# Kernel tuning notes

Measured on AMD Instinct MI355X. Metric: run time of the kernel, lower is better.

The kernel has to match this reference:

```python
import jax, jax.numpy as jnp
from jax import lax
import numpy as np

INPUT_SIZE = 128
T = 64
B = 8192
HIDDENS = [32, 16, 8]
FUTURE = 1


def _lstm_layer(x, w_ih, w_hh, b_ih, b_hh):
    """PyTorch-semantics single-layer LSTM, batch_first, zero init state.
    x: [B,T,D]; w_ih: [4H,D]; w_hh: [4H,H]; b_ih,b_hh: [4H]. Gate order i,f,g,o.
    Returns all hidden states [B,T,H]."""
    Bsz = x.shape[0]
    H = w_hh.shape[1]
    # Precompute input contribution for all timesteps in one big GEMM.
    xg = jnp.einsum('btd,gd->btg', x, w_ih) + b_ih + b_hh  # [B,T,4H]
    xg_t = jnp.swapaxes(xg, 0, 1)  # [T,B,4H]

    def step(carry, xt):
        h, c = carry
        gates = xt + h @ w_hh.T  # [B,4H]
        i, f, g, o = jnp.split(gates, 4, axis=-1)
        i = jax.nn.sigmoid(i)
        f = jax.nn.sigmoid(f)
        g = jnp.tanh(g)
        o = jax.nn.sigmoid(o)
        c = f * c + i * g
        h = o * jnp.tanh(c)
        return (h, c), h

    init = (jnp.zeros((Bsz, H), x.dtype), jnp.zeros((Bsz, H), x.dtype))
    _, hs = lax.scan(step, init, xg_t)  # hs: [T,B,H]
    return jnp.swapaxes(hs, 0, 1)


def setup_inputs() -> dict:
    key = jax.random.key(0)
    ks = jax.random.split(key, 16)
    s = 0.1

    def rn(k, shape):
        return jax.random.normal(k, shape, dtype=jnp.float32) * s

    inp = {
        'x': jax.random.normal(ks[0], (B, T, INPUT_SIZE), dtype=jnp.float32),
        'w_ih1': rn(ks[1], (4 * 32, INPUT_SIZE)),
        'w_hh1': rn(ks[2], (4 * 32, 32)),
        'b_ih1': rn(ks[3], (4 * 32,)),
        'b_hh1': rn(ks[4], (4 * 32,)),
        'w_ih2': rn(ks[5], (4 * 16, 32)),
        'w_hh2': rn(ks[6], (4 * 16, 16)),
        'b_ih2': rn(ks[7], (4 * 16,)),
        'b_hh2': rn(ks[8], (4 * 16,)),
        'w_ih3': rn(ks[9], (4 * 8, 16)),
        'w_hh3': rn(ks[10], (4 * 8, 8)),
        'b_ih3': rn(ks[11], (4 * 8,)),
        'b_hh3': rn(ks[12], (4 * 8,)),
        'fc_w': rn(ks[13], (FUTURE, 8)),
        'fc_b': rn(ks[14], (FUTURE,)),
    }
    return inp


def reference(x, w_ih1, w_hh1, b_ih1, b_hh1, w_ih2, w_hh2, b_ih2, b_hh2,
              w_ih3, w_hh3, b_ih3, b_hh3, fc_w, fc_b):
    h = _lstm_layer(x, w_ih1, w_hh1, b_ih1, b_hh1)   # [B,T,32]
    h = _lstm_layer(h, w_ih2, w_hh2, b_ih2, b_hh2)   # [B,T,16]
    h = _lstm_layer(h, w_ih3, w_hh3, b_ih3, b_hh3)   # [B,T,8]
    return h[:, -1, :] @ fc_w.T + fc_b               # [B, FUTURE]
```

## Files before the change

### kernel.cpp

```cpp
#include <hip/hip_runtime.h>
#include <cstddef>
#include <type_traits>


typedef _Float16 h8_t  __attribute__((ext_vector_type(8)));
typedef _Float16 h4_t  __attribute__((ext_vector_type(4)));
typedef __fp16   p2_t  __attribute__((ext_vector_type(2)));
typedef float    f4_t  __attribute__((ext_vector_type(4)));

#define T_LEN 64
#define D_IN  128

__device__ __forceinline__ float sig_(float x)  { return 1.0f / (1.0f + __expf(-x)); }
__device__ __forceinline__ float tanh_(float x) { float e = __expf(2.0f * x); return 1.0f - 2.0f / (e + 1.0f); }

__device__ __forceinline__ h8_t zero8h() {
    h8_t r = { (_Float16)0.f,(_Float16)0.f,(_Float16)0.f,(_Float16)0.f,
               (_Float16)0.f,(_Float16)0.f,(_Float16)0.f,(_Float16)0.f };
    return r;
}
__device__ __forceinline__ h8_t cvt8(f4_t lo, f4_t hi) {
    union { h8_t v8; p2_t v2[4]; } u;
    u.v2[0] = __builtin_amdgcn_cvt_pkrtz(lo[0], lo[1]);
    u.v2[1] = __builtin_amdgcn_cvt_pkrtz(lo[2], lo[3]);
    u.v2[2] = __builtin_amdgcn_cvt_pkrtz(hi[0], hi[1]);
    u.v2[3] = __builtin_amdgcn_cvt_pkrtz(hi[2], hi[3]);
    return u.v8;
}
__device__ __forceinline__ h4_t cvt4(f4_t v) {
    union { h4_t v4; p2_t v2[2]; } u;
    u.v2[0] = __builtin_amdgcn_cvt_pkrtz(v[0], v[1]);
    u.v2[1] = __builtin_amdgcn_cvt_pkrtz(v[2], v[3]);
    return u.v4;
}
__device__ __forceinline__ h8_t load8f_h(const float* __restrict__ p) {
    f4_t lo = *(const f4_t*)p, hi = *(const f4_t*)(p + 4);
    return cvt8(lo, hi);
}

__device__ __forceinline__ void bar_lds() {
    asm volatile("s_waitcnt lgkmcnt(0)" ::: "memory");
    __builtin_amdgcn_s_barrier();
}

__global__ __launch_bounds__(512, 4)
void lstm_one(const float* __restrict__ x,
              const float* __restrict__ w_ih1, const float* __restrict__ w_hh1,
              const float* __restrict__ b_ih1, const float* __restrict__ b_hh1,
              const float* __restrict__ w_ih2, const float* __restrict__ w_hh2,
              const float* __restrict__ b_ih2, const float* __restrict__ b_hh2,
              const float* __restrict__ w_ih3, const float* __restrict__ w_hh3,
              const float* __restrict__ b_ih3, const float* __restrict__ b_hh3,
              const float* __restrict__ fc_w, const float* __restrict__ fc_b,
              float* __restrict__ out)
{
    __shared__ __align__(16) _Float16 h1s[2][16][40];
    __shared__ __align__(16) _Float16 h2s[2][16][24];
    __shared__ __align__(16) _Float16 h3s[2][16][8];
    __shared__ __align__(16) _Float16 xs[2][16 * 128];

    const int tid  = threadIdx.x;
    const int lane = tid & 63;
    const int wid8 = tid >> 6;
    const int w    = wid8 & 3;
    const int rsel = wid8 >> 2;
    const int nl = lane & 15, qd = lane >> 4;
    const int n7 = nl & 7;
    const bool lo8 = (nl & 8) == 0;

    h8_t bw1[2][4], bh1[2];
    #pragma unroll
    for (int j = 0; j < 2; ++j) {
        int G = 8 * w + n7 + 32 * ((nl >> 3) + 2 * j);
        #pragma unroll
        for (int kc = 0; kc < 4; ++kc)
            bw1[j][kc] = load8f_h(w_ih1 + G * 128 + kc * 32 + qd * 8);
        bh1[j] = load8f_h(w_hh1 + G * 32 + qd * 8);
    }
    h8_t bw2[2] = {zero8h(), zero8h()}, bh2[2] = {zero8h(), zero8h()};
    float bs2[4] = {0.f, 0.f, 0.f, 0.f};
    if (w < 2) {
        #pragma unroll
        for (int j = 0; j < 2; ++j) {
            int G = 32 * j + 16 * (nl >> 3) + 8 * w + n7;
            bw2[j] = load8f_h(w_ih2 + G * 32 + qd * 8);
            bh2[j] = (qd < 2) ? load8f_h(w_hh2 + G * 16 + qd * 8) : zero8h();
        }
        int u2 = 8 * w + n7;
        #pragma unroll
        for (int g = 0; g < 4; ++g) bs2[g] = b_ih2[16 * g + u2] + b_hh2[16 * g + u2];
    }
    h8_t b3c[2] = {zero8h(), zero8h()};
    float bs3[4] = {0.f, 0.f, 0.f, 0.f};
    if (wid8 == 2 || wid8 == 3) {
        #pragma unroll
        for (int j = 0; j < 2; ++j) {
            int G = 16 * j + 8 * (nl >> 3) + n7;
            b3c[j] = (qd < 2) ? load8f_h(w_ih3 + G * 16 + qd * 8)
                   : (qd == 2) ? load8f_h(w_hh3 + G * 8) : zero8h();
        }
        #pragma unroll
        for (int g = 0; g < 4; ++g) bs3[g] = b_ih3[8 * g + n7] + b_hh3[8 * g + n7];
    }
    float bs1[4];
    {
        int u1 = 8 * w + n7;
        #pragma unroll
        for (int g = 0; g < 4; ++g) bs1[g] = b_ih1[32 * g + u1] + b_hh1[32 * g + u1];
    }

    for (int i = tid; i < 2 * 16 * 40; i += 512) (&h1s[0][0][0])[i] = (_Float16)0.f;
    for (int i = tid; i < 2 * 16 * 24; i += 512) (&h2s[0][0][0])[i] = (_Float16)0.f;
    for (int i = tid; i < 2 * 16 * 8;  i += 512) (&h3s[0][0][0])[i] = (_Float16)0.f;

    float c1 = 0.f;
    float c2 = 0.f;
    float c3 = 0.f;

    const int b0 = blockIdx.x * 16;

    const int xrow = tid >> 5, xch = (tid >> 1) & 15, xh = tid & 1;
    const float* xg = x + ((size_t)(b0 + xrow) * T_LEN) * D_IN + xch * 8 + xh * 4;
    const int xws = (xrow * 16 + (xch ^ (xrow & 7))) * 8 + xh * 4;

    f4_t xa = *(const f4_t*)xg;
    *(h4_t*)&xs[0][xws] = cvt4(xa);
    xa = *(const f4_t*)(xg + D_IN);
    __syncthreads();

    auto step = [&](auto d1c, auto d2c, auto d3c, auto pc, int t) {
        constexpr bool DO1 = decltype(d1c)::value;
        constexpr bool DO2 = decltype(d2c)::value;
        constexpr bool DO3 = decltype(d3c)::value;
        constexpr int  P   = decltype(pc)::value;

        h8_t a1p = zero8h();
        if constexpr (DO1 || DO2)
            a1p = *(const h8_t*)&h1s[1 - P][nl][qd * 8];

        if constexpr (DO1) {
            h8_t af[4];
            #pragma unroll
            for (int kc = 0; kc < 4; ++kc)
                af[kc] = *(const h8_t*)&xs[P][(nl * 16 + ((4 * kc + qd) ^ n7)) * 8];

            h4_t xcur = cvt4(xa);
            {
                int tn = (t + 2 < T_LEN) ? (t + 2) : (T_LEN - 1);
                xa = *(const f4_t*)(xg + tn * D_IN);
            }
            *(h4_t*)&xs[1 - P][xws] = xcur;

            f4_t acc[2];
            #pragma unroll
            for (int j = 0; j < 2; ++j) {
                f4_t a_ = {0.f, 0.f, 0.f, 0.f};
                #pragma unroll
                for (int kc = 0; kc < 4; ++kc)
                    a_ = __builtin_amdgcn_mfma_f32_16x16x32_f16(af[kc], bw1[j][kc], a_, 0, 0, 0);
                a_ = __builtin_amdgcn_mfma_f32_16x16x32_f16(a1p, bh1[j], a_, 0, 0, 0);
                acc[j] = a_;
            }
            auto ew1 = [&](auto rrc) {
                constexpr int rr = decltype(rrc)::value;
                float s0 = lo8 ? acc[0][rr + 2] : acc[0][rr];
                float s1 = lo8 ? acc[1][rr + 2] : acc[1][rr];
                float x0 = __shfl_xor(s0, 8, 64);
                float x1 = __shfl_xor(s1, 8, 64);
                float vi = lo8 ? acc[0][rr] : x0;
                float vf = lo8 ? x0 : acc[0][rr + 2];
                float vg = lo8 ? acc[1][rr] : x1;
                float vo = lo8 ? x1 : acc[1][rr + 2];
                float ig = sig_(vi + bs1[0]);
                float fg = sig_(vf + bs1[1]);
                float gg = tanh_(vg + bs1[2]);
                float og = sig_(vo + bs1[3]);
                float c = fg * c1 + ig * gg; c1 = c;
                float h = og * tanh_(c);
                h1s[P][4 * qd + rr + (lo8 ? 0 : 2)][8 * w + n7] = (_Float16)h;
            };
            if (rsel == 0) ew1(std::integral_constant<int, 0>{});
            else           ew1(std::integral_constant<int, 1>{});
        }

        if constexpr (DO2) {
            if (w < 2) {
                h8_t a2p = zero8h();
                if (qd < 2) a2p = *(const h8_t*)&h2s[P][nl][qd * 8];
                f4_t acc2[2];
                #pragma unroll
                for (int j = 0; j < 2; ++j) {
                    f4_t a_ = {0.f, 0.f, 0.f, 0.f};
                    a_ = __builtin_amdgcn_mfma_f32_16x16x32_f16(a1p, bw2[j], a_, 0, 0, 0);
                    a_ = __builtin_amdgcn_mfma_f32_16x16x32_f16(a2p, bh2[j], a_, 0, 0, 0);
                    acc2[j] = a_;
                }
                auto ew2 = [&](auto rrc) {
                    constexpr int rr = decltype(rrc)::value;
                    float s0 = lo8 ? acc2[0][rr + 2] : acc2[0][rr];
                    float s1 = lo8 ? acc2[1][rr + 2] : acc2[1][rr];
                    float x0 = __shfl_xor(s0, 8, 64);
                    float x1 = __shfl_xor(s1, 8, 64);
                    float vi = lo8 ? acc2[0][rr] : x0;
                    float vf = lo8 ? x0 : acc2[0][rr + 2];
                    float vg = lo8 ? acc2[1][rr] : x1;
                    float vo = lo8 ? x1 : acc2[1][rr + 2];
                    float ig = sig_(vi + bs2[0]);
                    float fg = sig_(vf + bs2[1]);
                    float gg = tanh_(vg + bs2[2]);
                    float og = sig_(vo + bs2[3]);
                    float c = fg * c2 + ig * gg; c2 = c;
                    float h = og * tanh_(c);
                    h2s[1 - P][4 * qd + rr + (lo8 ? 0 : 2)][8 * w + n7] = (_Float16)h;
                };
                if (rsel == 0) ew2(std::integral_constant<int, 0>{});
                else           ew2(std::integral_constant<int, 1>{});
            }
        }

        if constexpr (DO3) {
            if (wid8 == 2 || wid8 == 3) {
                h8_t a3 = zero8h();
                if (qd < 2)       a3 = *(const h8_t*)&h2s[P][nl][qd * 8];
                else if (qd == 2) a3 = *(const h8_t*)&h3s[1 - P][nl][0];
                f4_t acc3[2];
                #pragma unroll
                for (int j = 0; j < 2; ++j) {
                    f4_t a_ = {0.f, 0.f, 0.f, 0.f};
                    acc3[j] = __builtin_amdgcn_mfma_f32_16x16x32_f16(a3, b3c[j], a_, 0, 0, 0);
                }
                auto l3c = [&](auto rpc) {
                    constexpr int rp = decltype(rpc)::value;
                    float eLo = acc3[0][rp], eHi = acc3[0][rp + 2];
                    float oLo = acc3[1][rp], oHi = acc3[1][rp + 2];
                    float se = lo8 ? eHi : eLo; float xe = __shfl_xor(se, 8, 64);
                    float so = lo8 ? oHi : oLo; float xo = __shfl_xor(so, 8, 64);
                    float vi = lo8 ? eLo : xe;
                    float vf = lo8 ? xe  : eHi;
                    float vg = lo8 ? oLo : xo;
                    float vo = lo8 ? xo  : oHi;
                    float ig = sig_(vi + bs3[0]);
                    float fg = sig_(vf + bs3[1]);
                    float gg = tanh_(vg + bs3[2]);
                    float og = sig_(vo + bs3[3]);
                    float c = fg * c3 + ig * gg; c3 = c;
                    float h = og * tanh_(c);
                    h3s[P][4 * qd + rp + (lo8 ? 0 : 2)][n7] = (_Float16)h;
                };
                if (wid8 == 2) l3c(std::integral_constant<int, 0>{});
                else           l3c(std::integral_constant<int, 1>{});
            }
        }

        bar_lds();
    };

    using TT = std::integral_constant<bool, true>;
    using FF = std::integral_constant<bool, false>;
    using P0 = std::integral_constant<int, 0>;
    using P1 = std::integral_constant<int, 1>;

    step(TT{}, FF{}, FF{}, P0{}, 0);
    step(TT{}, TT{}, FF{}, P1{}, 1);
    for (int tb = 1; tb < 32; ++tb) {
        step(TT{}, TT{}, TT{}, P0{}, 2 * tb);
        step(TT{}, TT{}, TT{}, P1{}, 2 * tb + 1);
    }
    step(FF{}, TT{}, TT{}, P0{}, 64);
    step(FF{}, FF{}, TT{}, P1{}, 65);

    if (tid < 16) {
        float a = fc_b[0];
        #pragma unroll
        for (int u = 0; u < 8; ++u)
            a += fc_w[u] * (float)h3s[1][tid][u];
        out[b0 + tid] = a;
    }
}

extern "C" void kernel_launch(void* const* d_in, const int* in_sizes, int n_in,
                              void* d_out, int out_size, void* d_ws, size_t ws_size,
                              hipStream_t stream) {
    (void)in_sizes; (void)n_in; (void)out_size; (void)d_ws; (void)ws_size;
    const float* x     = (const float*)d_in[0];
    const float* w_ih1 = (const float*)d_in[1];
    const float* w_hh1 = (const float*)d_in[2];
    const float* b_ih1 = (const float*)d_in[3];
    const float* b_hh1 = (const float*)d_in[4];
    const float* w_ih2 = (const float*)d_in[5];
    const float* w_hh2 = (const float*)d_in[6];
    const float* b_ih2 = (const float*)d_in[7];
    const float* b_hh2 = (const float*)d_in[8];
    const float* w_ih3 = (const float*)d_in[9];
    const float* w_hh3 = (const float*)d_in[10];
    const float* b_ih3 = (const float*)d_in[11];
    const float* b_hh3 = (const float*)d_in[12];
    const float* fc_w  = (const float*)d_in[13];
    const float* fc_b  = (const float*)d_in[14];

    dim3 grid(512), block(512);
    hipLaunchKernelGGL(lstm_one, grid, block, 0, stream,
                       x, w_ih1, w_hh1, b_ih1, b_hh1,
                       w_ih2, w_hh2, b_ih2, b_hh2,
                       w_ih3, w_hh3, b_ih3, b_hh3,
                       fc_w, fc_b, (float*)d_out);
}
```

Measured before the change: 457.9 us.

## Share layer-2/3 weight and state registers across waves and relax launch bounds

Waves 0-1 (w<2) run layer 2 and waves 2-3 run layer 3, so the two groups never overlap. The change merges their per-wave weight fragments, bias and cell-state registers into one shared set, cutting live register use. It also lowers the launch-bounds minimum from 4 to 2 blocks per CU, which gives the compiler a larger register budget and can reduce spilling, at the cost of possibly lower occupancy.

```diff
diff --git a/kernel.cpp b/kernel.cpp
--- a/kernel.cpp
+++ b/kernel.cpp
@@ -43,7 +43,7 @@
     __builtin_amdgcn_s_barrier();
 }
 
-__global__ __launch_bounds__(512, 4)
+__global__ __launch_bounds__(512, 2)
 void lstm_one(const float* __restrict__ x,
               const float* __restrict__ w_ih1, const float* __restrict__ w_hh1,
               const float* __restrict__ b_ih1, const float* __restrict__ b_hh1,
@@ -77,30 +77,27 @@
             bw1[j][kc] = load8f_h(w_ih1 + G * 128 + kc * 32 + qd * 8);
         bh1[j] = load8f_h(w_hh1 + G * 32 + qd * 8);
     }
-    h8_t bw2[2] = {zero8h(), zero8h()}, bh2[2] = {zero8h(), zero8h()};
-    float bs2[4] = {0.f, 0.f, 0.f, 0.f};
+    h8_t bwX[2] = {zero8h(), zero8h()}, bhX[2] = {zero8h(), zero8h()};
+    float bsX[4] = {0.f, 0.f, 0.f, 0.f};
     if (w < 2) {
         #pragma unroll
         for (int j = 0; j < 2; ++j) {
             int G = 32 * j + 16 * (nl >> 3) + 8 * w + n7;
-            bw2[j] = load8f_h(w_ih2 + G * 32 + qd * 8);
-            bh2[j] = (qd < 2) ? load8f_h(w_hh2 + G * 16 + qd * 8) : zero8h();
+            bwX[j] = load8f_h(w_ih2 + G * 32 + qd * 8);
+            bhX[j] = (qd < 2) ? load8f_h(w_hh2 + G * 16 + qd * 8) : zero8h();
         }
         int u2 = 8 * w + n7;
         #pragma unroll
-        for (int g = 0; g < 4; ++g) bs2[g] = b_ih2[16 * g + u2] + b_hh2[16 * g + u2];
-    }
-    h8_t b3c[2] = {zero8h(), zero8h()};
-    float bs3[4] = {0.f, 0.f, 0.f, 0.f};
-    if (wid8 == 2 || wid8 == 3) {
+        for (int g = 0; g < 4; ++g) bsX[g] = b_ih2[16 * g + u2] + b_hh2[16 * g + u2];
+    } else if (wid8 == 2 || wid8 == 3) {
         #pragma unroll
         for (int j = 0; j < 2; ++j) {
             int G = 16 * j + 8 * (nl >> 3) + n7;
-            b3c[j] = (qd < 2) ? load8f_h(w_ih3 + G * 16 + qd * 8)
+            bwX[j] = (qd < 2) ? load8f_h(w_ih3 + G * 16 + qd * 8)
                    : (qd == 2) ? load8f_h(w_hh3 + G * 8) : zero8h();
         }
         #pragma unroll
-        for (int g = 0; g < 4; ++g) bs3[g] = b_ih3[8 * g + n7] + b_hh3[8 * g + n7];
+        for (int g = 0; g < 4; ++g) bsX[g] = b_ih3[8 * g + n7] + b_hh3[8 * g + n7];
     }
     float bs1[4];
     {
@@ -114,8 +111,7 @@
     for (int i = tid; i < 2 * 16 * 8;  i += 512) (&h3s[0][0][0])[i] = (_Float16)0.f;
 
     float c1 = 0.f;
-    float c2 = 0.f;
-    float c3 = 0.f;
+    float cX = 0.f;
 
     const int b0 = blockIdx.x * 16;
 
@@ -191,8 +187,8 @@
                 #pragma unroll
                 for (int j = 0; j < 2; ++j) {
                     f4_t a_ = {0.f, 0.f, 0.f, 0.f};
-                    a_ = __builtin_amdgcn_mfma_f32_16x16x32_f16(a1p, bw2[j], a_, 0, 0, 0);
-                    a_ = __builtin_amdgcn_mfma_f32_16x16x32_f16(a2p, bh2[j], a_, 0, 0, 0);
+                    a_ = __builtin_amdgcn_mfma_f32_16x16x32_f16(a1p, bwX[j], a_, 0, 0, 0);
+                    a_ = __builtin_amdgcn_mfma_f32_16x16x32_f16(a2p, bhX[j], a_, 0, 0, 0);
                     acc2[j] = a_;
                 }
                 auto ew2 = [&](auto rrc) {
@@ -205,11 +201,11 @@
                     float vf = lo8 ? x0 : acc2[0][rr + 2];
                     float vg = lo8 ? acc2[1][rr] : x1;
                     float vo = lo8 ? x1 : acc2[1][rr + 2];
-                    float ig = sig_(vi + bs2[0]);
-                    float fg = sig_(vf + bs2[1]);
-                    float gg = tanh_(vg + bs2[2]);
-                    float og = sig_(vo + bs2[3]);
-                    float c = fg * c2 + ig * gg; c2 = c;
+                    float ig = sig_(vi + bsX[0]);
+                    float fg = sig_(vf + bsX[1]);
+                    float gg = tanh_(vg + bsX[2]);
+                    float og = sig_(vo + bsX[3]);
+                    float c = fg * cX + ig * gg; cX = c;
                     float h = og * tanh_(c);
                     h2s[1 - P][4 * qd + rr + (lo8 ? 0 : 2)][8 * w + n7] = (_Float16)h;
                 };
@@ -227,7 +223,7 @@
                 #pragma unroll
                 for (int j = 0; j < 2; ++j) {
                     f4_t a_ = {0.f, 0.f, 0.f, 0.f};
-                    acc3[j] = __builtin_amdgcn_mfma_f32_16x16x32_f16(a3, b3c[j], a_, 0, 0, 0);
+                    acc3[j] = __builtin_amdgcn_mfma_f32_16x16x32_f16(a3, bwX[j], a_, 0, 0, 0);
                 }
                 auto l3c = [&](auto rpc) {
                     constexpr int rp = decltype(rpc)::value;
@@ -239,11 +235,11 @@
                     float vf = lo8 ? xe  : eHi;
                     float vg = lo8 ? oLo : xo;
                     float vo = lo8 ? xo  : oHi;
-                    float ig = sig_(vi + bs3[0]);
-                    float fg = sig_(vf + bs3[1]);
-                    float gg = tanh_(vg + bs3[2]);
-                    float og = sig_(vo + bs3[3]);
-                    float c = fg * c3 + ig * gg; c3 = c;
+                    float ig = sig_(vi + bsX[0]);
+                    float fg = sig_(vf + bsX[1]);
+                    float gg = tanh_(vg + bsX[2]);
+                    float og = sig_(vo + bsX[3]);
+                    float c = fg * cX + ig * gg; cX = c;
                     float h = og * tanh_(c);
                     h3s[P][4 * qd + rp + (lo8 ? 0 : 2)][n7] = (_Float16)h;
                 };
```

New measurement: 454.6 us. About the same (-0.7%).
